# Kernel tuning notes

Measured on AMD Instinct MI355X. Metric: run time of the kernel, lower is better.

The kernel has to match this reference:

```python
import jax, jax.numpy as jnp
import numpy as np

# db4 decomposition filters (pywt convention)
DB4_LO = np.array([-0.010597401784997278, 0.032883011666982945, 0.030841381835986965,
                   -0.18703481171888114, -0.02798376941698385, 0.6308807679295904,
                   0.7148465705525415, 0.23037781330885523], dtype=np.float32)
DB4_HI = np.array([-0.23037781330885523, 0.7148465705525415, -0.6308807679295904,
                   -0.02798376941698385, 0.18703481171888114, 0.030841381835986965,
                   -0.032883011666982945, -0.010597401784997278], dtype=np.float32)
PAD = 3


def setup_inputs() -> dict:
    key = jax.random.key(0)
    x = jax.random.normal(key, (4, 3, 32, 256, 256), dtype=jnp.float32)
    filt = jnp.stack([jnp.asarray(DB4_LO), jnp.asarray(DB4_HI)])  # [2, 8]
    return {"x": x, "filt": filt}


def _dwt1d(x, filt, axis):
    """Analysis filter bank along one axis: reflect-pad, true convolution
    with (dec_lo, dec_hi), stride 2. Returns (low, high) with that axis halved."""
    x = jnp.moveaxis(x, axis, -1)
    shp = x.shape
    L = shp[-1]
    x2 = x.reshape(-1, 1, L)
    x2 = jnp.pad(x2, ((0, 0), (0, 0), (PAD, PAD)), mode="reflect")
    # flip filters so lax correlation == mathematical convolution with dec filters
    k = jnp.flip(filt, axis=-1)[:, None, :]  # [2, 1, 8]
    y = jax.lax.conv_general_dilated(
        x2, k, window_strides=(2,), padding="VALID",
        dimension_numbers=("NCH", "OIH", "NCH"))  # [N, 2, L//2]
    y = y.reshape(shp[:-1] + (2, L // 2))
    lo = jnp.moveaxis(y[..., 0, :], -1, axis)
    hi = jnp.moveaxis(y[..., 1, :], -1, axis)
    return lo, hi


def reference(x, filt):
    # x: [B, C, T, H, W] -> [B, 8C, T/2, H/2, W/2]
    lo_t, hi_t = _dwt1d(x, filt, 2)
    subbands = []
    for a in (lo_t, hi_t):
        lo_h, hi_h = _dwt1d(a, filt, 3)
        for b in (lo_h, hi_h):
            lo_w, hi_w = _dwt1d(b, filt, 4)
            subbands.append(lo_w)
            subbands.append(hi_w)
    # order: LLL, LLH, LHL, LHH, HLL, HLH, HHL, HHH (t,h,w)
    return jnp.concatenate(subbands, axis=1)
```

## Files before the change

kernel.cpp:

```cpp
#include <hip/hip_runtime.h>
#include <hip/hip_bf16.h>


#define CC 3
#define TT 32
#define HH 256
#define WW 256
#define TOH 16
#define HOH 128
#define WOH 128

#define TH 4
#define TW 32
#define NROWS 14
#define RSLOT 72
#define RSLOT2 36
#define NSLOTS 8
#define DEPTH 6
#define NW 8
#define NTHREADS 512
#define VSTR 512
#define NRR (4*NROWS)
#define NIT (NRR/2)

constexpr float GLO[8] = {
     0.23037781330885523f,  0.7148465705525415f,   0.6308807679295904f,
    -0.02798376941698385f, -0.18703481171888114f,  0.030841381835986965f,
     0.032883011666982945f, -0.010597401784997278f };
constexpr float GHI[8] = {
    -0.010597401784997278f, -0.032883011666982945f, 0.030841381835986965f,
     0.18703481171888114f,  -0.02798376941698385f,  -0.6308807679295904f,
     0.7148465705525415f,   -0.23037781330885523f };

__device__ __forceinline__ int refl(int p, int n) {
    p = p < 0 ? -p : p;
    p = p >= n ? 2 * n - 2 - p : p;
    return p;
}

__global__ __launch_bounds__(NTHREADS)
void dwt3d_db4_kernel(const float* __restrict__ x, float* __restrict__ out) {
    __shared__ float Ring[NW * NSLOTS * RSLOT];
    __shared__ __hip_bfloat16 Vbuf[TT * VSTR];

    const int tid  = threadIdx.x;
    const int wid  = tid >> 6;
    const int lane = tid & 63;
    const int wo   = lane & 31;
    const int p    = lane >> 5;

    const int lin = blockIdx.x;
    const int nid = (lin & 7) * 192 + (lin >> 3);
    const int wo0 = (nid & 3) * TW;
    const int ho0 = ((nid >> 2) & 31) * TH;
    const int bz  = nid >> 7;
    const int b = bz / CC, c = bz - b * CC;

    const float* xs = x + (size_t)bz * (TT * HH * WW);

    const int gcol0 = refl(2 * wo0 - 3 + lane, WW);
    const int gcol1 = refl(2 * wo0 + 3 + lane, WW);

    float wH0[4], wH1[4];
#pragma unroll
    for (int d = 0; d < 4; ++d) {
        wH0[d] = p ? GLO[2 * d + 1] : GLO[2 * d];
        wH1[d] = p ? GHI[2 * d + 1] : GHI[2 * d];
    }

    const int t0 = wid * 4;
    const int ringbase = wid * (NSLOTS * RSLOT);
    const float2* Ring2 = (const float2*)Ring;
    const int r2base = wid * (NSLOTS * RSLOT2) + p * RSLOT2 + wo;
    const int vcolbase = p * 128 + wo;

#define ISSUE(rr_) do {                                                       \
        const int t_ = (rr_) / NROWS, r_ = (rr_) % NROWS;                     \
        const int gr_ = refl(2 * ho0 - 3 + r_, HH);                           \
        const float* rowp_ = xs + (size_t)(t0 + t_) * (HH * WW) + gr_ * WW;   \
        float* lp_ = &Ring[ringbase + ((rr_) & (NSLOTS - 1)) * RSLOT];        \
        __builtin_amdgcn_global_load_lds(                                     \
            (const __attribute__((address_space(1))) void*)(rowp_ + gcol0),   \
            (__attribute__((address_space(3))) void*)lp_, 4, 0, 0);           \
        __builtin_amdgcn_global_load_lds(                                     \
            (const __attribute__((address_space(1))) void*)(rowp_ + gcol1),   \
            (__attribute__((address_space(3))) void*)(lp_ + 6), 4, 0, 0);     \
    } while (0)

    float vacc0[2][4], vacc1[2][4];
#pragma unroll
    for (int sh = 0; sh < 2; ++sh)
#pragma unroll
        for (int ho = 0; ho < 4; ++ho) { vacc0[sh][ho] = 0.f; vacc1[sh][ho] = 0.f; }

#pragma unroll
    for (int rr = 0; rr < DEPTH; ++rr) ISSUE(rr);

#pragma unroll
    for (int k = 0; k < NIT; ++k) {
        if (k <= 25)      asm volatile("s_waitcnt vmcnt(8)" ::: "memory");
        else if (k == 26) asm volatile("s_waitcnt vmcnt(4)" ::: "memory");
        else              asm volatile("s_waitcnt vmcnt(0)" ::: "memory");

        const int soff = ((2 * k) & (NSLOTS - 1)) * RSLOT2;
        const float2 d0 = Ring2[r2base + soff + 0];
        const float2 d1 = Ring2[r2base + soff + 1];
        const float2 d2 = Ring2[r2base + soff + 2];
        const float2 d3 = Ring2[r2base + soff + 3];

        float m_lo, m_hi;
        {
            float a0 = d0.x, a1 = d0.y, a2 = d1.x, a3 = d1.y;
            float a4 = d2.x, a5 = d2.y, a6 = d3.x, a7 = d3.y;
            m_lo = a0 * GLO[0]; m_hi = a0 * GHI[0];
            m_lo = fmaf(a1, GLO[1], m_lo); m_hi = fmaf(a1, GHI[1], m_hi);
            m_lo = fmaf(a2, GLO[2], m_lo); m_hi = fmaf(a2, GHI[2], m_hi);
            m_lo = fmaf(a3, GLO[3], m_lo); m_hi = fmaf(a3, GHI[3], m_hi);
            m_lo = fmaf(a4, GLO[4], m_lo); m_hi = fmaf(a4, GHI[4], m_hi);
            m_lo = fmaf(a5, GLO[5], m_lo); m_hi = fmaf(a5, GHI[5], m_hi);
            m_lo = fmaf(a6, GLO[6], m_lo); m_hi = fmaf(a6, GHI[6], m_hi);
            m_lo = fmaf(a7, GLO[7], m_lo); m_hi = fmaf(a7, GHI[7], m_hi);
        }

        if (2 * k + 6 < NRR) { ISSUE(2 * k + 6); ISSUE(2 * k + 7); }

        const int kk = k % 7;
#pragma unroll
        for (int ho = 0; ho < 4; ++ho) {
            const int d = kk - ho;
            if (d >= 0 && d < 4) {
                vacc0[0][ho] = fmaf(m_lo, wH0[d], vacc0[0][ho]);
                vacc0[1][ho] = fmaf(m_lo, wH1[d], vacc0[1][ho]);
                vacc1[0][ho] = fmaf(m_hi, wH0[d], vacc1[0][ho]);
                vacc1[1][ho] = fmaf(m_hi, wH1[d], vacc1[1][ho]);
            }
        }

        if (kk == 6) {
            const int t = t0 + k / 7;
#pragma unroll
            for (int sh = 0; sh < 2; ++sh)
#pragma unroll
                for (int ho = 0; ho < 4; ++ho) {
                    const float send = p ? vacc0[sh][ho] : vacc1[sh][ho];
                    const float keep = p ? vacc1[sh][ho] : vacc0[sh][ho];
                    const float recv = __shfl_xor(send, 32, 64);
                    Vbuf[t * VSTR + sh * 256 + vcolbase + ho * 32] =
                        __float2bfloat16(keep + recv);
                    vacc0[sh][ho] = 0.f; vacc1[sh][ho] = 0.f;
                }
        }
    }

    __syncthreads();

    float v[TT];
#pragma unroll
    for (int t = 0; t < TT; ++t) v[t] = __bfloat162float(Vbuf[t * VSTR + tid]);

    const int subhw = tid >> 7;
    const int hoq   = (tid >> 5) & 3;
    const int wo2   = tid & 31;

    const size_t hw = (size_t)(ho0 + hoq) * WOH + (wo0 + wo2);
    const size_t ch_lo = (size_t)(subhw * CC + c);
    const size_t ch_hi = (size_t)((4 + subhw) * CC + c);
    const size_t o_lo = (((size_t)b * 24 + ch_lo) * TOH) * (HOH * WOH) + hw;
    const size_t o_hi = (((size_t)b * 24 + ch_hi) * TOH) * (HOH * WOH) + hw;

#pragma unroll
    for (int to = 0; to < TOH; ++to) {
        float lo = 0.f, hi = 0.f;
#pragma unroll
        for (int j = 0; j < 8; ++j) {
            int q = 2 * to + j - 3;
            q = q < 0 ? -q : q;
            q = q >= TT ? 2 * TT - 2 - q : q;
            lo = fmaf(v[q], GLO[j], lo);
            hi = fmaf(v[q], GHI[j], hi);
        }
        out[o_lo + (size_t)to * (HOH * WOH)] = lo;
        out[o_hi + (size_t)to * (HOH * WOH)] = hi;
    }
}

extern "C" void kernel_launch(void* const* d_in, const int* in_sizes, int n_in,
                              void* d_out, int out_size, void* d_ws, size_t ws_size,
                              hipStream_t stream) {
    (void)in_sizes; (void)n_in; (void)d_ws; (void)ws_size; (void)out_size;
    const float* x = (const float*)d_in[0];
    float* out = (float*)d_out;
    dim3 grid(1536, 1, 1);
    dim3 block(NTHREADS);
    hipLaunchKernelGGL(dwt3d_db4_kernel, grid, block, 0, stream, x, out);
}
```

Baseline: 43.87 us.

## Use 16-byte LDS-direct loads and halve intermediate LDS buffer for higher occupancy

After: 89.21 us. +103.3%, slower.

```diff
diff --git a/kernel.cpp b/kernel.cpp
--- a/kernel.cpp
+++ b/kernel.cpp
@@ -9,19 +9,10 @@
 #define TOH 16
 #define HOH 128
 #define WOH 128
-
 #define TH 4
 #define TW 32
 #define NROWS 14
-#define RSLOT 72
-#define RSLOT2 36
-#define NSLOTS 8
-#define DEPTH 6
-#define NW 8
 #define NTHREADS 512
-#define VSTR 512
-#define NRR (4*NROWS)
-#define NIT (NRR/2)
 
 constexpr float GLO[8] = {
      0.23037781330885523f,  0.7148465705525415f,   0.6308807679295904f,
@@ -38,10 +29,20 @@
     return p;
 }
 
-__global__ __launch_bounds__(NTHREADS)
+__device__ __forceinline__ unsigned short f2bfbits(float f) {
+    __hip_bfloat16 h = __float2bfloat16(f);
+    return reinterpret_cast<unsigned short&>(h);
+}
+__device__ __forceinline__ __hip_bfloat16 bits2bf(unsigned short u) {
+    __hip_bfloat16 h;
+    reinterpret_cast<unsigned short&>(h) = u;
+    return h;
+}
+
+__global__ __launch_bounds__(NTHREADS, 6)
 void dwt3d_db4_kernel(const float* __restrict__ x, float* __restrict__ out) {
-    __shared__ float Ring[NW * NSLOTS * RSLOT];
-    __shared__ __hip_bfloat16 Vbuf[TT * VSTR];
+    __shared__ float Ring[8 * 1152];
+    __shared__ __hip_bfloat16 Vbuf2[TT * 256];
 
     const int tid  = threadIdx.x;
     const int wid  = tid >> 6;
@@ -57,9 +58,53 @@
     const int b = bz / CC, c = bz - b * CC;
 
     const float* xs = x + (size_t)bz * (TT * HH * WW);
-
-    const int gcol0 = refl(2 * wo0 - 3 + lane, WW);
-    const int gcol1 = refl(2 * wo0 + 3 + lane, WW);
+    const int t0 = wid * 4;
+
+    const int cbase = 2 * wo0 - 4;
+    int lrow[2], scol[2], scol2;
+    {
+#pragma unroll
+        for (int q = 0; q < 2; ++q) {
+            const int u = 64 * q + lane;
+            const int lr = u / 18;
+            const int lc = u - 18 * lr;
+            lrow[q] = lr;
+            int sc = cbase + 4 * lc;
+            if (wo0 == 0  && lc == 0)  sc = 0;
+            if (wo0 == 96 && lc == 17) sc = 252;
+            scol[q] = sc;
+        }
+        int sc = cbase + 8 + lane;
+        if (wo0 == 96 && lane >= 60) sc = 192 + lane;
+        scol2 = sc;
+    }
+    float* const ringw = &Ring[wid * 1152];
+
+#define ISSUE_GROUP(g_) do {                                                  \
+        _Pragma("unroll")                                                     \
+        for (int q_ = 0; q_ < 2; ++q_) {                                      \
+            const int rr_ = 8 * (g_) + lrow[q_];                              \
+            const int tq_ = rr_ / NROWS, rq_ = rr_ - NROWS * tq_;             \
+            const int grow_ = refl(2 * ho0 - 3 + rq_, HH);                    \
+            const float* src_ = xs + (size_t)(t0 + tq_) * (HH * WW)           \
+                                + grow_ * WW + scol[q_];                      \
+            __builtin_amdgcn_global_load_lds(                                 \
+                (const __attribute__((address_space(1))) void*)src_,          \
+                (__attribute__((address_space(3))) void*)                     \
+                    (ringw + ((g_) & 1) * 576 + q_ * 256), 16, 0, 0);         \
+        }                                                                     \
+        {                                                                     \
+            const int rr_ = 8 * (g_) + 7;                                     \
+            const int tq_ = rr_ / NROWS, rq_ = rr_ - NROWS * tq_;             \
+            const int grow_ = refl(2 * ho0 - 3 + rq_, HH);                    \
+            const float* src_ = xs + (size_t)(t0 + tq_) * (HH * WW)           \
+                                + grow_ * WW + scol2;                         \
+            __builtin_amdgcn_global_load_lds(                                 \
+                (const __attribute__((address_space(1))) void*)src_,          \
+                (__attribute__((address_space(3))) void*)                     \
+                    (ringw + ((g_) & 1) * 576 + 512), 4, 0, 0);               \
+        }                                                                     \
+    } while (0)
 
     float wH0[4], wH1[4];
 #pragma unroll
@@ -68,24 +113,8 @@
         wH1[d] = p ? GHI[2 * d + 1] : GHI[2 * d];
     }
 
-    const int t0 = wid * 4;
-    const int ringbase = wid * (NSLOTS * RSLOT);
     const float2* Ring2 = (const float2*)Ring;
-    const int r2base = wid * (NSLOTS * RSLOT2) + p * RSLOT2 + wo;
-    const int vcolbase = p * 128 + wo;
-
-#define ISSUE(rr_) do {                                                       \
-        const int t_ = (rr_) / NROWS, r_ = (rr_) % NROWS;                     \
-        const int gr_ = refl(2 * ho0 - 3 + r_, HH);                           \
-        const float* rowp_ = xs + (size_t)(t0 + t_) * (HH * WW) + gr_ * WW;   \
-        float* lp_ = &Ring[ringbase + ((rr_) & (NSLOTS - 1)) * RSLOT];        \
-        __builtin_amdgcn_global_load_lds(                                     \
-            (const __attribute__((address_space(1))) void*)(rowp_ + gcol0),   \
-            (__attribute__((address_space(3))) void*)lp_, 4, 0, 0);           \
-        __builtin_amdgcn_global_load_lds(                                     \
-            (const __attribute__((address_space(1))) void*)(rowp_ + gcol1),   \
-            (__attribute__((address_space(3))) void*)(lp_ + 6), 4, 0, 0);     \
-    } while (0)
+    const int r2base = wid * 576 + wo;
 
     float vacc0[2][4], vacc1[2][4];
 #pragma unroll
@@ -93,36 +122,48 @@
 #pragma unroll
         for (int ho = 0; ho < 4; ++ho) { vacc0[sh][ho] = 0.f; vacc1[sh][ho] = 0.f; }
 
-#pragma unroll
-    for (int rr = 0; rr < DEPTH; ++rr) ISSUE(rr);
-
-#pragma unroll
-    for (int k = 0; k < NIT; ++k) {
-        if (k <= 25)      asm volatile("s_waitcnt vmcnt(8)" ::: "memory");
-        else if (k == 26) asm volatile("s_waitcnt vmcnt(4)" ::: "memory");
-        else              asm volatile("s_waitcnt vmcnt(0)" ::: "memory");
-
-        const int soff = ((2 * k) & (NSLOTS - 1)) * RSLOT2;
+    unsigned pkA[4], pkB[4];
+
+    ISSUE_GROUP(0);
+    ISSUE_GROUP(1);
+
+#pragma unroll
+    for (int k = 0; k < 28; ++k) {
+        if (k < 24) asm volatile("s_waitcnt vmcnt(3)" ::: "memory");
+        else        asm volatile("s_waitcnt vmcnt(0)" ::: "memory");
+
+        const int soff = ((k >> 2) & 1) * 288 + (k & 3) * 72 + p * 36;
         const float2 d0 = Ring2[r2base + soff + 0];
         const float2 d1 = Ring2[r2base + soff + 1];
         const float2 d2 = Ring2[r2base + soff + 2];
         const float2 d3 = Ring2[r2base + soff + 3];
+        const float2 d4 = Ring2[r2base + soff + 4];
+
+        float a0 = d0.y, a1 = d1.x, a2 = d1.y, a3 = d2.x;
+        float a4 = d2.y, a5 = d3.x, a6 = d3.y, a7 = d4.x;
+
+        if (wo0 == 0) {
+            if (wo == 0)      { a0 = d3.y; a1 = d3.x; a2 = d2.y; }
+            else if (wo == 1) { a0 = d1.y; }
+        } else if (wo0 == 96) {
+            if (wo == 30)      { a7 = d3.x; }
+            else if (wo == 31) { a5 = d2.x; a6 = d1.y; a7 = d1.x; }
+        }
 
         float m_lo, m_hi;
-        {
-            float a0 = d0.x, a1 = d0.y, a2 = d1.x, a3 = d1.y;
-            float a4 = d2.x, a5 = d2.y, a6 = d3.x, a7 = d3.y;
-            m_lo = a0 * GLO[0]; m_hi = a0 * GHI[0];
-            m_lo = fmaf(a1, GLO[1], m_lo); m_hi = fmaf(a1, GHI[1], m_hi);
-            m_lo = fmaf(a2, GLO[2], m_lo); m_hi = fmaf(a2, GHI[2], m_hi);
-            m_lo = fmaf(a3, GLO[3], m_lo); m_hi = fmaf(a3, GHI[3], m_hi);
-            m_lo = fmaf(a4, GLO[4], m_lo); m_hi = fmaf(a4, GHI[4], m_hi);
-            m_lo = fmaf(a5, GLO[5], m_lo); m_hi = fmaf(a5, GHI[5], m_hi);
-            m_lo = fmaf(a6, GLO[6], m_lo); m_hi = fmaf(a6, GHI[6], m_hi);
-            m_lo = fmaf(a7, GLO[7], m_lo); m_hi = fmaf(a7, GHI[7], m_hi);
-        }
-
-        if (2 * k + 6 < NRR) { ISSUE(2 * k + 6); ISSUE(2 * k + 7); }
+        m_lo = a0 * GLO[0]; m_hi = a0 * GHI[0];
+        m_lo = fmaf(a1, GLO[1], m_lo); m_hi = fmaf(a1, GHI[1], m_hi);
+        m_lo = fmaf(a2, GLO[2], m_lo); m_hi = fmaf(a2, GHI[2], m_hi);
+        m_lo = fmaf(a3, GLO[3], m_lo); m_hi = fmaf(a3, GHI[3], m_hi);
+        m_lo = fmaf(a4, GLO[4], m_lo); m_hi = fmaf(a4, GHI[4], m_hi);
+        m_lo = fmaf(a5, GLO[5], m_lo); m_hi = fmaf(a5, GHI[5], m_hi);
+        m_lo = fmaf(a6, GLO[6], m_lo); m_hi = fmaf(a6, GHI[6], m_hi);
+        m_lo = fmaf(a7, GLO[7], m_lo); m_hi = fmaf(a7, GHI[7], m_hi);
+
+        if (((k & 3) == 3) && k <= 19) {
+            __builtin_amdgcn_sched_barrier(0);
+            ISSUE_GROUP((k >> 2) + 2);
+        }
 
         const int kk = k % 7;
 #pragma unroll
@@ -137,51 +178,95 @@
         }
 
         if (kk == 6) {
-            const int t = t0 + k / 7;
-#pragma unroll
-            for (int sh = 0; sh < 2; ++sh)
-#pragma unroll
-                for (int ho = 0; ho < 4; ++ho) {
-                    const float send = p ? vacc0[sh][ho] : vacc1[sh][ho];
-                    const float keep = p ? vacc1[sh][ho] : vacc0[sh][ho];
+            const int t  = t0 + k / 7;
+            const int si = k / 7;
+            unsigned w0 = 0, w1 = 0;
+#pragma unroll
+            for (int ho = 0; ho < 4; ++ho) {
+                {
+                    const float send = p ? vacc0[0][ho] : vacc1[0][ho];
+                    const float keep = p ? vacc1[0][ho] : vacc0[0][ho];
                     const float recv = __shfl_xor(send, 32, 64);
-                    Vbuf[t * VSTR + sh * 256 + vcolbase + ho * 32] =
+                    Vbuf2[t * 256 + p * 128 + ho * 32 + wo] =
                         __float2bfloat16(keep + recv);
-                    vacc0[sh][ho] = 0.f; vacc1[sh][ho] = 0.f;
                 }
+                {
+                    const float send = p ? vacc0[1][ho] : vacc1[1][ho];
+                    const float keep = p ? vacc1[1][ho] : vacc0[1][ho];
+                    const float recv = __shfl_xor(send, 32, 64);
+                    const unsigned us = f2bfbits(keep + recv);
+                    if (ho == 0) w0 = us;
+                    if (ho == 1) w0 |= us << 16;
+                    if (ho == 2) w1 = us;
+                    if (ho == 3) w1 |= us << 16;
+                }
+                vacc0[0][ho] = 0.f; vacc0[1][ho] = 0.f;
+                vacc1[0][ho] = 0.f; vacc1[1][ho] = 0.f;
+            }
+            pkA[si] = w0; pkB[si] = w1;
         }
     }
 
     __syncthreads();
 
-    float v[TT];
-#pragma unroll
-    for (int t = 0; t < TT; ++t) v[t] = __bfloat162float(Vbuf[t * VSTR + tid]);
-
-    const int subhw = tid >> 7;
-    const int hoq   = (tid >> 5) & 3;
-    const int wo2   = tid & 31;
-
-    const size_t hw = (size_t)(ho0 + hoq) * WOH + (wo0 + wo2);
-    const size_t ch_lo = (size_t)(subhw * CC + c);
-    const size_t ch_hi = (size_t)((4 + subhw) * CC + c);
-    const size_t o_lo = (((size_t)b * 24 + ch_lo) * TOH) * (HOH * WOH) + hw;
-    const size_t o_hi = (((size_t)b * 24 + ch_hi) * TOH) * (HOH * WOH) + hw;
-
-#pragma unroll
-    for (int to = 0; to < TOH; ++to) {
-        float lo = 0.f, hi = 0.f;
-#pragma unroll
-        for (int j = 0; j < 8; ++j) {
-            int q = 2 * to + j - 3;
-            q = q < 0 ? -q : q;
-            q = q >= TT ? 2 * TT - 2 - q : q;
-            lo = fmaf(v[q], GLO[j], lo);
-            hi = fmaf(v[q], GHI[j], hi);
-        }
-        out[o_lo + (size_t)to * (HOH * WOH)] = lo;
-        out[o_hi + (size_t)to * (HOH * WOH)] = hi;
-    }
+    const int colA = tid & 255;
+    const int tohalf = tid >> 8;
+    const int swT = colA >> 7, hoT = (colA >> 5) & 3, woT = colA & 31;
+    const size_t hwoff = (size_t)(ho0 + hoT) * WOH + (wo0 + woT);
+
+    float v[22];
+    if (tid < 256) {
+#pragma unroll
+        for (int i = 0; i < 22; ++i)
+            v[i] = __bfloat162float(Vbuf2[refl(i - 3, TT) * 256 + colA]);
+    } else {
+#pragma unroll
+        for (int i = 0; i < 22; ++i)
+            v[i] = __bfloat162float(Vbuf2[refl(13 + i, TT) * 256 + colA]);
+    }
+    __syncthreads();
+
+#pragma unroll
+    for (int si = 0; si < 4; ++si) {
+        const int t = t0 + si;
+        const unsigned w0 = pkA[si], w1 = pkB[si];
+        Vbuf2[t * 256 + p * 128 + 0 * 32 + wo] = bits2bf((unsigned short)(w0 & 0xffff));
+        Vbuf2[t * 256 + p * 128 + 1 * 32 + wo] = bits2bf((unsigned short)(w0 >> 16));
+        Vbuf2[t * 256 + p * 128 + 2 * 32 + wo] = bits2bf((unsigned short)(w1 & 0xffff));
+        Vbuf2[t * 256 + p * 128 + 3 * 32 + wo] = bits2bf((unsigned short)(w1 >> 16));
+    }
+    __syncthreads();
+
+#define TCOMPUTE(sh_) do {                                                    \
+        const int ch_lo = (0 + 2 * (sh_) + swT) * CC + c;                     \
+        const int ch_hi = (4 + 2 * (sh_) + swT) * CC + c;                     \
+        _Pragma("unroll")                                                     \
+        for (int tl = 0; tl < 8; ++tl) {                                      \
+            float lo = 0.f, hi = 0.f;                                         \
+            _Pragma("unroll")                                                 \
+            for (int j = 0; j < 8; ++j) {                                     \
+                const float vv = v[2 * tl + j];                               \
+                lo = fmaf(vv, GLO[j], lo);                                    \
+                hi = fmaf(vv, GHI[j], hi);                                    \
+            }                                                                 \
+            const int to = tohalf * 8 + tl;                                   \
+            out[((size_t)(b * 24 + ch_lo) * TOH + to) * (HOH * WOH) + hwoff] = lo; \
+            out[((size_t)(b * 24 + ch_hi) * TOH + to) * (HOH * WOH) + hwoff] = hi; \
+        }                                                                     \
+    } while (0)
+
+    TCOMPUTE(0);
+
+    if (tid < 256) {
+#pragma unroll
+        for (int i = 0; i < 22; ++i)
+            v[i] = __bfloat162float(Vbuf2[refl(i - 3, TT) * 256 + colA]);
+    } else {
+#pragma unroll
+        for (int i = 0; i < 22; ++i)
+            v[i] = __bfloat162float(Vbuf2[refl(13 + i, TT) * 256 + colA]);
+    }
+    TCOMPUTE(1);
 }
 
 extern "C" void kernel_launch(void* const* d_in, const int* in_sizes, int n_in,
```

## Switch row staging to 16-byte aligned global-to-LDS loads with edge fixups

Applied to the files above, without the earlier changes.

Result: slower. 49.60 us (+13.0%).

```diff
diff --git a/kernel.cpp b/kernel.cpp
--- a/kernel.cpp
+++ b/kernel.cpp
@@ -9,19 +9,12 @@
 #define TOH 16
 #define HOH 128
 #define WOH 128
-
 #define TH 4
 #define TW 32
 #define NROWS 14
-#define RSLOT 72
-#define RSLOT2 36
-#define NSLOTS 8
-#define DEPTH 6
-#define NW 8
 #define NTHREADS 512
 #define VSTR 512
-#define NRR (4*NROWS)
-#define NIT (NRR/2)
+#define RWAVE 544
 
 constexpr float GLO[8] = {
      0.23037781330885523f,  0.7148465705525415f,   0.6308807679295904f,
@@ -40,7 +33,7 @@
 
 __global__ __launch_bounds__(NTHREADS)
 void dwt3d_db4_kernel(const float* __restrict__ x, float* __restrict__ out) {
-    __shared__ float Ring[NW * NSLOTS * RSLOT];
+    __shared__ float Ring[8 * RWAVE];
     __shared__ __hip_bfloat16 Vbuf[TT * VSTR];
 
     const int tid  = threadIdx.x;
@@ -57,9 +50,30 @@
     const int b = bz / CC, c = bz - b * CC;
 
     const float* xs = x + (size_t)bz * (TT * HH * WW);
-
-    const int gcol0 = refl(2 * wo0 - 3 + lane, WW);
-    const int gcol1 = refl(2 * wo0 + 3 + lane, WW);
+    const int t0 = wid * 4;
+
+    const int cbase = 2 * wo0 - 4;
+    const int rowoff = lane / 18;
+    const int lcq = lane - 18 * rowoff;
+    int scol = cbase + 4 * lcq;
+    if (wo0 == 0  && lcq == 0)  scol = 0;
+    if (wo0 == 96 && lcq == 17) scol = 252;
+
+    float* const ringw = &Ring[wid * RWAVE];
+
+#define ISSUE(k_) do {                                                        \
+        int rr_ = 2 * (k_) + rowoff;                                          \
+        rr_ = rr_ > 55 ? 55 : rr_;             \
+        const int tq_ = (rr_ * 2341) >> 15;                \
+        const int rq_ = rr_ - 14 * tq_;                                       \
+        const int grow_ = refl(2 * ho0 - 3 + rq_, HH);                        \
+        const float* src_ = xs + (size_t)(t0 + tq_) * (HH * WW)               \
+                            + grow_ * WW + scol;                              \
+        __builtin_amdgcn_global_load_lds(                                     \
+            (const __attribute__((address_space(1))) void*)src_,              \
+            (__attribute__((address_space(3))) void*)                         \
+                (ringw + ((k_) % 3) * 144), 16, 0, 0);                        \
+    } while (0)
 
     float wH0[4], wH1[4];
 #pragma unroll
@@ -68,61 +82,53 @@
         wH1[d] = p ? GHI[2 * d + 1] : GHI[2 * d];
     }
 
-    const int t0 = wid * 4;
-    const int ringbase = wid * (NSLOTS * RSLOT);
     const float2* Ring2 = (const float2*)Ring;
-    const int r2base = wid * (NSLOTS * RSLOT2) + p * RSLOT2 + wo;
+    const int r2base = wid * (RWAVE / 2) + p * 36 + wo;
     const int vcolbase = p * 128 + wo;
 
-#define ISSUE(rr_) do {                                                       \
-        const int t_ = (rr_) / NROWS, r_ = (rr_) % NROWS;                     \
-        const int gr_ = refl(2 * ho0 - 3 + r_, HH);                           \
-        const float* rowp_ = xs + (size_t)(t0 + t_) * (HH * WW) + gr_ * WW;   \
-        float* lp_ = &Ring[ringbase + ((rr_) & (NSLOTS - 1)) * RSLOT];        \
-        __builtin_amdgcn_global_load_lds(                                     \
-            (const __attribute__((address_space(1))) void*)(rowp_ + gcol0),   \
-            (__attribute__((address_space(3))) void*)lp_, 4, 0, 0);           \
-        __builtin_amdgcn_global_load_lds(                                     \
-            (const __attribute__((address_space(1))) void*)(rowp_ + gcol1),   \
-            (__attribute__((address_space(3))) void*)(lp_ + 6), 4, 0, 0);     \
-    } while (0)
-
     float vacc0[2][4], vacc1[2][4];
 #pragma unroll
     for (int sh = 0; sh < 2; ++sh)
 #pragma unroll
         for (int ho = 0; ho < 4; ++ho) { vacc0[sh][ho] = 0.f; vacc1[sh][ho] = 0.f; }
 
-#pragma unroll
-    for (int rr = 0; rr < DEPTH; ++rr) ISSUE(rr);
-
-#pragma unroll
-    for (int k = 0; k < NIT; ++k) {
-        if (k <= 25)      asm volatile("s_waitcnt vmcnt(8)" ::: "memory");
-        else if (k == 26) asm volatile("s_waitcnt vmcnt(4)" ::: "memory");
-        else              asm volatile("s_waitcnt vmcnt(0)" ::: "memory");
-
-        const int soff = ((2 * k) & (NSLOTS - 1)) * RSLOT2;
+    ISSUE(0);
+    ISSUE(1);
+
+#pragma unroll
+    for (int k = 0; k < 28; ++k) {
+        if (k <= 26) asm volatile("s_waitcnt vmcnt(1)" ::: "memory");
+        else         asm volatile("s_waitcnt vmcnt(0)" ::: "memory");
+
+        const int soff = (k % 3) * 72;
         const float2 d0 = Ring2[r2base + soff + 0];
         const float2 d1 = Ring2[r2base + soff + 1];
         const float2 d2 = Ring2[r2base + soff + 2];
         const float2 d3 = Ring2[r2base + soff + 3];
+        const float2 d4 = Ring2[r2base + soff + 4];
+
+        float a0 = d0.y, a1 = d1.x, a2 = d1.y, a3 = d2.x;
+        float a4 = d2.y, a5 = d3.x, a6 = d3.y, a7 = d4.x;
+
+        if (wo0 == 0) {
+            if (wo == 0)      { a0 = d3.y; a1 = d3.x; a2 = d2.y; }
+            else if (wo == 1) { a0 = d1.y; }
+        } else if (wo0 == 96) {
+            if (wo == 30)      { a7 = d3.x; }
+            else if (wo == 31) { a5 = d2.x; a6 = d1.y; a7 = d1.x; }
+        }
 
         float m_lo, m_hi;
-        {
-            float a0 = d0.x, a1 = d0.y, a2 = d1.x, a3 = d1.y;
-            float a4 = d2.x, a5 = d2.y, a6 = d3.x, a7 = d3.y;
-            m_lo = a0 * GLO[0]; m_hi = a0 * GHI[0];
-            m_lo = fmaf(a1, GLO[1], m_lo); m_hi = fmaf(a1, GHI[1], m_hi);
-            m_lo = fmaf(a2, GLO[2], m_lo); m_hi = fmaf(a2, GHI[2], m_hi);
-            m_lo = fmaf(a3, GLO[3], m_lo); m_hi = fmaf(a3, GHI[3], m_hi);
-            m_lo = fmaf(a4, GLO[4], m_lo); m_hi = fmaf(a4, GHI[4], m_hi);
-            m_lo = fmaf(a5, GLO[5], m_lo); m_hi = fmaf(a5, GHI[5], m_hi);
-            m_lo = fmaf(a6, GLO[6], m_lo); m_hi = fmaf(a6, GHI[6], m_hi);
-            m_lo = fmaf(a7, GLO[7], m_lo); m_hi = fmaf(a7, GHI[7], m_hi);
-        }
-
-        if (2 * k + 6 < NRR) { ISSUE(2 * k + 6); ISSUE(2 * k + 7); }
+        m_lo = a0 * GLO[0]; m_hi = a0 * GHI[0];
+        m_lo = fmaf(a1, GLO[1], m_lo); m_hi = fmaf(a1, GHI[1], m_hi);
+        m_lo = fmaf(a2, GLO[2], m_lo); m_hi = fmaf(a2, GHI[2], m_hi);
+        m_lo = fmaf(a3, GLO[3], m_lo); m_hi = fmaf(a3, GHI[3], m_hi);
+        m_lo = fmaf(a4, GLO[4], m_lo); m_hi = fmaf(a4, GHI[4], m_hi);
+        m_lo = fmaf(a5, GLO[5], m_lo); m_hi = fmaf(a5, GHI[5], m_hi);
+        m_lo = fmaf(a6, GLO[6], m_lo); m_hi = fmaf(a6, GHI[6], m_hi);
+        m_lo = fmaf(a7, GLO[7], m_lo); m_hi = fmaf(a7, GHI[7], m_hi);
+
+        if (k <= 25) ISSUE(k + 2);
 
         const int kk = k % 7;
 #pragma unroll
```

## Process two channel volumes per block and prefetch second during first epilogue

Applied to the files above, without the earlier changes.

New measurement: 45.57 us. 3.9% more time.

```diff
diff --git a/kernel.cpp b/kernel.cpp
--- a/kernel.cpp
+++ b/kernel.cpp
@@ -9,7 +9,6 @@
 #define TOH 16
 #define HOH 128
 #define WOH 128
-
 #define TH 4
 #define TW 32
 #define NROWS 14
@@ -17,11 +16,9 @@
 #define RSLOT2 36
 #define NSLOTS 8
 #define DEPTH 6
-#define NW 8
 #define NTHREADS 512
 #define VSTR 512
 #define NRR (4*NROWS)
-#define NIT (NRR/2)
 
 constexpr float GLO[8] = {
      0.23037781330885523f,  0.7148465705525415f,   0.6308807679295904f,
@@ -40,7 +37,7 @@
 
 __global__ __launch_bounds__(NTHREADS)
 void dwt3d_db4_kernel(const float* __restrict__ x, float* __restrict__ out) {
-    __shared__ float Ring[NW * NSLOTS * RSLOT];
+    __shared__ float Ring[8 * NSLOTS * RSLOT];
     __shared__ __hip_bfloat16 Vbuf[TT * VSTR];
 
     const int tid  = threadIdx.x;
@@ -50,13 +47,14 @@
     const int p    = lane >> 5;
 
     const int lin = blockIdx.x;
-    const int nid = (lin & 7) * 192 + (lin >> 3);
+    const int nid = (lin & 7) * 96 + (lin >> 3);
     const int wo0 = (nid & 3) * TW;
     const int ho0 = ((nid >> 2) & 31) * TH;
-    const int bz  = nid >> 7;
-    const int b = bz / CC, c = bz - b * CC;
+    const int g   = nid >> 7;
 
-    const float* xs = x + (size_t)bz * (TT * HH * WW);
+    const int t0 = wid * 4;
+    const float* const xs0 = x + (size_t)(2 * g)     * (TT * HH * WW);
+    const float* const xs1 = x + (size_t)(2 * g + 1) * (TT * HH * WW);
 
     const int gcol0 = refl(2 * wo0 - 3 + lane, WW);
     const int gcol1 = refl(2 * wo0 + 3 + lane, WW);
@@ -68,16 +66,15 @@
         wH1[d] = p ? GHI[2 * d + 1] : GHI[2 * d];
     }
 
-    const int t0 = wid * 4;
     const int ringbase = wid * (NSLOTS * RSLOT);
     const float2* Ring2 = (const float2*)Ring;
     const int r2base = wid * (NSLOTS * RSLOT2) + p * RSLOT2 + wo;
     const int vcolbase = p * 128 + wo;
 
-#define ISSUE(rr_) do {                                                       \
+#define ISSUE(xs_, rr_) do {                                                  \
         const int t_ = (rr_) / NROWS, r_ = (rr_) % NROWS;                     \
         const int gr_ = refl(2 * ho0 - 3 + r_, HH);                           \
-        const float* rowp_ = xs + (size_t)(t0 + t_) * (HH * WW) + gr_ * WW;   \
+        const float* rowp_ = (xs_) + (size_t)(t0 + t_) * (HH * WW) + gr_ * WW;\
         float* lp_ = &Ring[ringbase + ((rr_) & (NSLOTS - 1)) * RSLOT];        \
         __builtin_amdgcn_global_load_lds(                                     \
             (const __attribute__((address_space(1))) void*)(rowp_ + gcol0),   \
@@ -93,95 +90,101 @@
 #pragma unroll
         for (int ho = 0; ho < 4; ++ho) { vacc0[sh][ho] = 0.f; vacc1[sh][ho] = 0.f; }
 
-#pragma unroll
-    for (int rr = 0; rr < DEPTH; ++rr) ISSUE(rr);
+#define MAINLOOP(xs_) do {                                                    \
+    _Pragma("unroll")                                                         \
+    for (int k = 0; k < 28; ++k) {                                            \
+        if (k <= 25)      asm volatile("s_waitcnt vmcnt(8)" ::: "memory");    \
+        else if (k == 26) asm volatile("s_waitcnt vmcnt(4)" ::: "memory");    \
+        else              asm volatile("s_waitcnt vmcnt(0)" ::: "memory");    \
+        const int soff = ((2 * k) & (NSLOTS - 1)) * RSLOT2;                   \
+        const float2 d0 = Ring2[r2base + soff + 0];                           \
+        const float2 d1 = Ring2[r2base + soff + 1];                           \
+        const float2 d2 = Ring2[r2base + soff + 2];                           \
+        const float2 d3 = Ring2[r2base + soff + 3];                           \
+        float a0 = d0.x, a1 = d0.y, a2 = d1.x, a3 = d1.y;                     \
+        float a4 = d2.x, a5 = d2.y, a6 = d3.x, a7 = d3.y;                     \
+        float m_lo, m_hi;                                                     \
+        m_lo = a0 * GLO[0]; m_hi = a0 * GHI[0];                               \
+        m_lo = fmaf(a1, GLO[1], m_lo); m_hi = fmaf(a1, GHI[1], m_hi);         \
+        m_lo = fmaf(a2, GLO[2], m_lo); m_hi = fmaf(a2, GHI[2], m_hi);         \
+        m_lo = fmaf(a3, GLO[3], m_lo); m_hi = fmaf(a3, GHI[3], m_hi);         \
+        m_lo = fmaf(a4, GLO[4], m_lo); m_hi = fmaf(a4, GHI[4], m_hi);         \
+        m_lo = fmaf(a5, GLO[5], m_lo); m_hi = fmaf(a5, GHI[5], m_hi);         \
+        m_lo = fmaf(a6, GLO[6], m_lo); m_hi = fmaf(a6, GHI[6], m_hi);         \
+        m_lo = fmaf(a7, GLO[7], m_lo); m_hi = fmaf(a7, GHI[7], m_hi);         \
+        if (2 * k + 6 < NRR) { ISSUE(xs_, 2 * k + 6); ISSUE(xs_, 2 * k + 7); }\
+        const int kk = k % 7;                                                 \
+        _Pragma("unroll")                                                     \
+        for (int ho = 0; ho < 4; ++ho) {                                      \
+            const int d = kk - ho;                                            \
+            if (d >= 0 && d < 4) {                                            \
+                vacc0[0][ho] = fmaf(m_lo, wH0[d], vacc0[0][ho]);              \
+                vacc0[1][ho] = fmaf(m_lo, wH1[d], vacc0[1][ho]);              \
+                vacc1[0][ho] = fmaf(m_hi, wH0[d], vacc1[0][ho]);              \
+                vacc1[1][ho] = fmaf(m_hi, wH1[d], vacc1[1][ho]);              \
+            }                                                                 \
+        }                                                                     \
+        if (kk == 6) {                                                        \
+            const int t = t0 + k / 7;                                         \
+            _Pragma("unroll")                                                 \
+            for (int sh = 0; sh < 2; ++sh)                                    \
+                _Pragma("unroll")                                             \
+                for (int ho = 0; ho < 4; ++ho) {                              \
+                    const float send = p ? vacc0[sh][ho] : vacc1[sh][ho];     \
+                    const float keep = p ? vacc1[sh][ho] : vacc0[sh][ho];     \
+                    const float recv = __shfl_xor(send, 32, 64);              \
+                    Vbuf[t * VSTR + sh * 256 + vcolbase + ho * 32] =          \
+                        __float2bfloat16(keep + recv);                        \
+                    vacc0[sh][ho] = 0.f; vacc1[sh][ho] = 0.f;                 \
+                }                                                             \
+        }                                                                     \
+    }                                                                         \
+} while (0)
+
+#define TPHASE(bz_) do {                                                      \
+    float v[TT];                                                              \
+    _Pragma("unroll")                                                         \
+    for (int t = 0; t < TT; ++t)                                              \
+        v[t] = __bfloat162float(Vbuf[t * VSTR + tid]);                        \
+    const int b_ = (bz_) / CC, c_ = (bz_) - b_ * CC;                          \
+    const int subhw = tid >> 7;                                               \
+    const int hoq   = (tid >> 5) & 3;                                         \
+    const int wo2   = tid & 31;                                               \
+    const size_t hw = (size_t)(ho0 + hoq) * WOH + (wo0 + wo2);                \
+    const size_t ch_lo = (size_t)(subhw * CC + c_);                           \
+    const size_t ch_hi = (size_t)((4 + subhw) * CC + c_);                     \
+    const size_t o_lo = (((size_t)b_ * 24 + ch_lo) * TOH) * (HOH * WOH) + hw; \
+    const size_t o_hi = (((size_t)b_ * 24 + ch_hi) * TOH) * (HOH * WOH) + hw; \
+    _Pragma("unroll")                                                         \
+    for (int to = 0; to < TOH; ++to) {                                        \
+        float lo = 0.f, hi = 0.f;                                             \
+        _Pragma("unroll")                                                     \
+        for (int j = 0; j < 8; ++j) {                                         \
+            int q = 2 * to + j - 3;                                           \
+            q = q < 0 ? -q : q;                                               \
+            q = q >= TT ? 2 * TT - 2 - q : q;                                 \
+            lo = fmaf(v[q], GLO[j], lo);                                      \
+            hi = fmaf(v[q], GHI[j], hi);                                      \
+        }                                                                     \
+        out[o_lo + (size_t)to * (HOH * WOH)] = lo;                            \
+        out[o_hi + (size_t)to * (HOH * WOH)] = hi;                            \
+    }                                                                         \
+} while (0)
 
 #pragma unroll
-    for (int k = 0; k < NIT; ++k) {
-        if (k <= 25)      asm volatile("s_waitcnt vmcnt(8)" ::: "memory");
-        else if (k == 26) asm volatile("s_waitcnt vmcnt(4)" ::: "memory");
-        else              asm volatile("s_waitcnt vmcnt(0)" ::: "memory");
+    for (int rr = 0; rr < DEPTH; ++rr) ISSUE(xs0, rr);
+    MAINLOOP(xs0);
 
-        const int soff = ((2 * k) & (NSLOTS - 1)) * RSLOT2;
-        const float2 d0 = Ring2[r2base + soff + 0];
-        const float2 d1 = Ring2[r2base + soff + 1];
-        const float2 d2 = Ring2[r2base + soff + 2];
-        const float2 d3 = Ring2[r2base + soff + 3];
-
-        float m_lo, m_hi;
-        {
-            float a0 = d0.x, a1 = d0.y, a2 = d1.x, a3 = d1.y;
-            float a4 = d2.x, a5 = d2.y, a6 = d3.x, a7 = d3.y;
-            m_lo = a0 * GLO[0]; m_hi = a0 * GHI[0];
-            m_lo = fmaf(a1, GLO[1], m_lo); m_hi = fmaf(a1, GHI[1], m_hi);
-            m_lo = fmaf(a2, GLO[2], m_lo); m_hi = fmaf(a2, GHI[2], m_hi);
-            m_lo = fmaf(a3, GLO[3], m_lo); m_hi = fmaf(a3, GHI[3], m_hi);
-            m_lo = fmaf(a4, GLO[4], m_lo); m_hi = fmaf(a4, GHI[4], m_hi);
-            m_lo = fmaf(a5, GLO[5], m_lo); m_hi = fmaf(a5, GHI[5], m_hi);
-            m_lo = fmaf(a6, GLO[6], m_lo); m_hi = fmaf(a6, GHI[6], m_hi);
-            m_lo = fmaf(a7, GLO[7], m_lo); m_hi = fmaf(a7, GHI[7], m_hi);
-        }
-
-        if (2 * k + 6 < NRR) { ISSUE(2 * k + 6); ISSUE(2 * k + 7); }
-
-        const int kk = k % 7;
 #pragma unroll
-        for (int ho = 0; ho < 4; ++ho) {
-            const int d = kk - ho;
-            if (d >= 0 && d < 4) {
-                vacc0[0][ho] = fmaf(m_lo, wH0[d], vacc0[0][ho]);
-                vacc0[1][ho] = fmaf(m_lo, wH1[d], vacc0[1][ho]);
-                vacc1[0][ho] = fmaf(m_hi, wH0[d], vacc1[0][ho]);
-                vacc1[1][ho] = fmaf(m_hi, wH1[d], vacc1[1][ho]);
-            }
-        }
-
-        if (kk == 6) {
-            const int t = t0 + k / 7;
-#pragma unroll
-            for (int sh = 0; sh < 2; ++sh)
-#pragma unroll
-                for (int ho = 0; ho < 4; ++ho) {
-                    const float send = p ? vacc0[sh][ho] : vacc1[sh][ho];
-                    const float keep = p ? vacc1[sh][ho] : vacc0[sh][ho];
-                    const float recv = __shfl_xor(send, 32, 64);
-                    Vbuf[t * VSTR + sh * 256 + vcolbase + ho * 32] =
-                        __float2bfloat16(keep + recv);
-                    vacc0[sh][ho] = 0.f; vacc1[sh][ho] = 0.f;
-                }
-        }
-    }
+    for (int rr = 0; rr < DEPTH; ++rr) ISSUE(xs1, rr);
 
     __syncthreads();
+    TPHASE(2 * g);
+    __syncthreads();
 
-    float v[TT];
-#pragma unroll
-    for (int t = 0; t < TT; ++t) v[t] = __bfloat162float(Vbuf[t * VSTR + tid]);
-
-    const int subhw = tid >> 7;
-    const int hoq   = (tid >> 5) & 3;
-    const int wo2   = tid & 31;
-
-    const size_t hw = (size_t)(ho0 + hoq) * WOH + (wo0 + wo2);
-    const size_t ch_lo = (size_t)(subhw * CC + c);
-    const size_t ch_hi = (size_t)((4 + subhw) * CC + c);
-    const size_t o_lo = (((size_t)b * 24 + ch_lo) * TOH) * (HOH * WOH) + hw;
-    const size_t o_hi = (((size_t)b * 24 + ch_hi) * TOH) * (HOH * WOH) + hw;
-
-#pragma unroll
-    for (int to = 0; to < TOH; ++to) {
-        float lo = 0.f, hi = 0.f;
-#pragma unroll
-        for (int j = 0; j < 8; ++j) {
-            int q = 2 * to + j - 3;
-            q = q < 0 ? -q : q;
-            q = q >= TT ? 2 * TT - 2 - q : q;
-            lo = fmaf(v[q], GLO[j], lo);
-            hi = fmaf(v[q], GHI[j], hi);
-        }
-        out[o_lo + (size_t)to * (HOH * WOH)] = lo;
-        out[o_hi + (size_t)to * (HOH * WOH)] = hi;
-    }
+    MAINLOOP(xs1);
+    __syncthreads();
+    TPHASE(2 * g + 1);
 }
 
 extern "C" void kernel_launch(void* const* d_in, const int* in_sizes, int n_in,
@@ -190,7 +193,7 @@
     (void)in_sizes; (void)n_in; (void)d_ws; (void)ws_size; (void)out_size;
     const float* x = (const float*)d_in[0];
     float* out = (float*)d_out;
-    dim3 grid(1536, 1, 1);
+    dim3 grid(768, 1, 1);
     dim3 block(NTHREADS);
     hipLaunchKernelGGL(dwt3d_db4_kernel, grid, block, 0, stream, x, out);
 }
```
